# Performance work log

Hardware: AMD Instinct MI355X
Metric: run time of the kernel (lower is better)

## Reference

```python
import jax, jax.numpy as jnp
import numpy as np

B, C, M, NH, F_, W = 2, 8, 8, 8, 1024, 512  # batch, channels, attention_maps, heads, features, frames
HD = F_ // NH
EXP = 4


def _conv(x, w, b):
    y = jax.lax.conv_general_dilated(x, w, (1, 1), 'SAME',
                                     dimension_numbers=('NCHW', 'OIHW', 'NCHW'))
    return y + b[None, :, None, None]


def _rope(x):
    # x: (..., seq, d); lucidrains-style interleaved rotary embedding
    d, n = x.shape[-1], x.shape[-2]
    inv = 1.0 / (10000.0 ** (jnp.arange(0, d, 2, dtype=jnp.float32) / d))
    fr = jnp.repeat(jnp.arange(n, dtype=jnp.float32)[:, None] * inv[None, :], 2, axis=-1)
    cos, sin = jnp.cos(fr), jnp.sin(fr)
    xr = jnp.stack((-x[..., 1::2], x[..., 0::2]), axis=-1).reshape(x.shape)
    return x * cos + xr * sin


def _mcln(x, w, b, eps=1e-5):
    # MultichannelLayerNorm: normalize over features axis (axis=2 of B,C,F,W)
    mu = jnp.mean(x, axis=2, keepdims=True)
    var = jnp.var(x, axis=2, keepdims=True)
    return (x - mu) / jnp.sqrt(var + eps) * w[None, :, :, None] + b[None, :, :, None]


def _mclin(x, w_pw):
    # MultichannelLinear positionwise: per-channel matmul over features
    return jnp.einsum('bcfw,cgf->bcgw', x, w_pw)


def setup_inputs() -> dict:
    key = jax.random.key(0)
    ks = jax.random.split(key, 24)
    s = 0.02
    d = {
        'x': jax.random.normal(ks[0], (B, C, F_, W), jnp.float32),
        'prev_qk': jax.random.normal(ks[1], (B, M, NH, W, W), jnp.float32),
        'qconv_w': jax.random.normal(ks[2], (M, C, 3, 3), jnp.float32) * s,
        'qconv_b': jnp.zeros((M,), jnp.float32),
        'q_pw': jax.random.normal(ks[3], (M, F_, F_), jnp.float32) * s,
        'kconv_w': jax.random.normal(ks[4], (M, C, 3, 3), jnp.float32) * s,
        'kconv_b': jnp.zeros((M,), jnp.float32),
        'k_pw': jax.random.normal(ks[5], (M, F_, F_), jnp.float32) * s,
        'vconv_w': jax.random.normal(ks[6], (M, C, 3, 3), jnp.float32) * s,
        'vconv_b': jnp.zeros((M,), jnp.float32),
        'v_pw': jax.random.normal(ks[7], (M, F_, F_), jnp.float32) * s,
        'o_pw': jax.random.normal(ks[8], (M, F_, F_), jnp.float32) * s,
        'o_dw': jax.random.normal(ks[9], (M, M), jnp.float32) * s,
        'oproj_w': jax.random.normal(ks[10], (C, C + M, 3, 3), jnp.float32) * s,
        'oproj_b': jnp.zeros((C,), jnp.float32),
        'n1_w': jnp.ones((C, F_), jnp.float32),
        'n1_b': jnp.zeros((C, F_), jnp.float32),
        'c1_w': jax.random.normal(ks[11], (C * EXP, C, 3, 3), jnp.float32) * s,
        'c1_b': jnp.zeros((C * EXP,), jnp.float32),
        'c2_w': jax.random.normal(ks[12], (C, C * EXP, 3, 3), jnp.float32) * s,
        'c2_b': jnp.zeros((C,), jnp.float32),
        'n2_w': jnp.ones((C, F_), jnp.float32),
        'n2_b': jnp.zeros((C, F_), jnp.float32),
    }
    return d


def _encoder(x, prev_qk, qconv_w, qconv_b, q_pw, kconv_w, kconv_b, k_pw,
             vconv_w, vconv_b, v_pw, o_pw, o_dw, oproj_w, oproj_b,
             n1_w, n1_b, c1_w, c1_b, c2_w, c2_b, n2_w, n2_b):
    b, c, h, w = x.shape

    def heads(y):  # (B,M,F,W) -> (B,M,NH,W,HD)
        return y.transpose(0, 1, 3, 2).reshape(b, M, w, NH, HD).transpose(0, 1, 3, 2, 4)

    q = _rope(heads(_mclin(_conv(x, qconv_w, qconv_b), q_pw)))
    k = _rope(heads(_mclin(_conv(x, kconv_w, kconv_b), k_pw)))
    v = heads(_mclin(_conv(x, vconv_w, vconv_b), v_pw))

    qk = jnp.einsum('bmnqd,bmnkd->bmnqk', q, k) / jnp.sqrt(jnp.float32(h))
    qk = qk + prev_qk
    a = jnp.einsum('bmnqk,bmnkd->bmnqd', jax.nn.softmax(qk, axis=-1), v)
    a = a.transpose(0, 1, 3, 2, 4).reshape(b, M, w, NH * HD).transpose(0, 1, 3, 2)  # (B,M,F,W)
    a = jnp.einsum('bcfw,dc->bdfw', _mclin(a, o_pw), o_dw)  # depthwise o_linear
    z = _conv(jnp.concatenate((x, a), axis=1), oproj_w, oproj_b)

    hid = _mcln(x + z, n1_w, n1_b)  # dropout is identity in eval
    z2 = _conv(jax.nn.gelu(_conv(hid, c1_w, c1_b), approximate=False), c2_w, c2_b)
    out = _mcln(hid + z2, n2_w, n2_b)
    return out, qk


def reference(x, prev_qk, qconv_w, qconv_b, q_pw, kconv_w, kconv_b, k_pw,
              vconv_w, vconv_b, v_pw, o_pw, o_dw, oproj_w, oproj_b,
              n1_w, n1_b, c1_w, c1_b, c2_w, c2_b, n2_w, n2_b):
    out, qk = _encoder(x, prev_qk, qconv_w, qconv_b, q_pw, kconv_w, kconv_b, k_pw,
                       vconv_w, vconv_b, v_pw, o_pw, o_dw, oproj_w, oproj_b,
                       n1_w, n1_b, c1_w, c1_b, c2_w, c2_b, n2_w, n2_b)
    return (out, out, qk)
```

## Files before the change

### kernel.cpp

```cpp
#include <hip/hip_runtime.h>
#include <math.h>

#define B_ 2
#define C_ 8
#define M_ 8
#define NH_ 8
#define F_ 1024
#define W_ 512
#define HD_ 128
#define FW 524288L
#define PF_ 1026
#define PW_ 514

typedef __bf16 bf16_t;
typedef __bf16 bf16x8 __attribute__((ext_vector_type(8)));
typedef __bf16 bf16x4 __attribute__((ext_vector_type(4)));
typedef float f32x4 __attribute__((ext_vector_type(4)));

__device__ __forceinline__ void gload16(const void* g, void* l) {
    __builtin_amdgcn_global_load_lds(
        (const __attribute__((address_space(1))) unsigned int*)g,
        (__attribute__((address_space(3))) unsigned int*)l,
        16, 0, 0);
}

__device__ __forceinline__ float gelu_f(float v) {
    return 0.5f * v * (1.0f + erff(v * 0.70710678118f));
}

__global__ __launch_bounds__(256)
void pad_stage_k(const float* __restrict__ x, bf16_t* __restrict__ px)
{
    long i = (long)blockIdx.x * 256 + threadIdx.x;
    if (i >= (long)B_ * PF_ * PW_) return;
    int wc = (int)(i % PW_);
    long t = i / PW_;
    int fr = (int)(t % PF_);
    int b  = (int)(t / PF_);
    bf16x8 v = {};
    if (fr >= 1 && fr <= F_ && wc >= 1 && wc <= W_) {
        const float* s = x + (long)b * 8 * FW + (long)(fr - 1) * W_ + (wc - 1);
        #pragma unroll
        for (int c = 0; c < 8; ++c) v[c] = (bf16_t)s[c * FW];
    }
    *(bf16x8*)&px[i * 8] = v;
}

__global__ __launch_bounds__(256)
void borderz8_k(bf16_t* __restrict__ p8a, bf16_t* __restrict__ p8b)
{
    int i = blockIdx.x * 256 + threadIdx.x;
    if (i >= 2 * 3076) return;
    int b = i / 3076, p = i % 3076;
    int fr, wc;
    if (p < 514)       { fr = 0;    wc = p; }
    else if (p < 1028) { fr = 1025; wc = p - 514; }
    else if (p < 2052) { fr = 1 + (p - 1028); wc = 0; }
    else               { fr = 1 + (p - 2052); wc = 513; }
    long pix = ((long)b * PF_ + fr) * PW_ + wc;
    bf16x8 z = {};
    *(bf16x8*)&p8a[pix * 8] = z;
    *(bf16x8*)&p8b[pix * 8] = z;
}

__global__ __launch_bounds__(256)
void borderz32_k(bf16_t* __restrict__ p32)
{
    int i = blockIdx.x * 256 + threadIdx.x;
    if (i >= 2 * 3076) return;
    int b = i / 3076, p = i % 3076;
    int fr, wc;
    if (p < 514)       { fr = 0;    wc = p; }
    else if (p < 1028) { fr = 1025; wc = p - 514; }
    else if (p < 2052) { fr = 1 + (p - 1028); wc = 0; }
    else               { fr = 1 + (p - 2052); wc = 513; }
    long pix = ((long)b * PF_ + fr) * PW_ + wc;
    bf16x8 z = {};
    #pragma unroll
    for (int k = 0; k < 4; ++k) *(bf16x8*)&p32[pix * 32 + k * 8] = z;
}

__global__ void aprep_k(const float* __restrict__ qw, const float* __restrict__ kw,
                        const float* __restrict__ vw, const float* __restrict__ ow,
                        const float* __restrict__ c1w, const float* __restrict__ c2w,
                        const float* __restrict__ qb, const float* __restrict__ kb,
                        const float* __restrict__ vb,
                        bf16_t* __restrict__ a_qkv, bf16_t* __restrict__ a_op,
                        bf16_t* __restrict__ a_c1, bf16_t* __restrict__ a_c2,
                        float* __restrict__ bias_qkv)
{
    int mode = blockIdx.y;
    int i = blockIdx.x * 256 + threadIdx.x;
    if (mode == 0) {
        if (i < 3072) {
            int k = i & 31, co = (i >> 5) & 31, df = i >> 10;
            int tap = k >> 3, ci = k & 7;
            float v = 0.f;
            if (tap < 3) {
                if (co < 8)       v = qw[((co * 8 + ci) * 3 + df) * 3 + tap];
                else if (co < 16) v = kw[(((co - 8) * 8 + ci) * 3 + df) * 3 + tap];
                else if (co < 24) v = vw[(((co - 16) * 8 + ci) * 3 + df) * 3 + tap];
            }
            a_qkv[i] = (bf16_t)v;
        }
        if (i < 32) bias_qkv[i] = (i < 8) ? qb[i] : (i < 16) ? kb[i - 8] : (i < 24) ? vb[i - 16] : 0.f;
    } else if (mode == 1) {
        if (i < 3072) {
            int k = i & 63, co = (i >> 6) & 15, df = i >> 10;
            int src = k >> 5, r = k & 31, tap = r >> 3, ci = src * 8 + (r & 7);
            float v = 0.f;
            if (co < 8 && tap < 3) v = ow[((co * 16 + ci) * 3 + df) * 3 + tap];
            a_op[i] = (bf16_t)v;
        }
    } else if (mode == 2) {
        if (i < 3072) {
            int k = i & 31, co = (i >> 5) & 31, df = i >> 10;
            int tap = k >> 3, ci = k & 7;
            float v = (tap < 3) ? c1w[((co * 8 + ci) * 3 + df) * 3 + tap] : 0.f;
            a_c1[i] = (bf16_t)v;
        }
    } else {
        if (i < 4608) {
            int k = i % 96, co = (i / 96) & 15, df = i / (96 * 16);
            int tap = k >> 5, ci = k & 31;
            float v = (co < 8) ? c2w[((co * 32 + ci) * 3 + df) * 3 + tap] : 0.f;
            a_c2[i] = (bf16_t)v;
        }
    }
}

template<int CIN, int KSTEPS, int MFRAGS, int DUAL, int EPI>
__global__ __launch_bounds__(256)
void convg_k(const bf16_t* __restrict__ px0, const bf16_t* __restrict__ px1,
             const bf16_t* __restrict__ Ab, const float* __restrict__ bias,
             const float* __restrict__ resid, void* __restrict__ outp)
{
    const int f = blockIdx.y, b = blockIdx.z;
    const int tid = threadIdx.x, lane = tid & 63, wid = tid >> 6;
    const int l15 = lane & 15, l4 = lane >> 4;
    const int wbase = blockIdx.x * 256 + wid * 64;
    const int KW = KSTEPS * 32, M16 = MFRAGS * 16;

    bf16x8 af[3][MFRAGS][KSTEPS];
    #pragma unroll
    for (int df = 0; df < 3; ++df)
        #pragma unroll
        for (int mf = 0; mf < MFRAGS; ++mf)
            #pragma unroll
            for (int kk = 0; kk < KSTEPS; ++kk)
                af[df][mf][kk] = *(const bf16x8*)&Ab[(long)(df * M16 + mf * 16 + l15) * KW + kk * 32 + l4 * 8];

    f32x4 acc[MFRAGS][4];
    #pragma unroll
    for (int mf = 0; mf < MFRAGS; ++mf)
        #pragma unroll
        for (int nf = 0; nf < 4; ++nf)
            acc[mf][nf] = (f32x4){0.f, 0.f, 0.f, 0.f};

    #pragma unroll
    for (int df = 0; df < 3; ++df) {
        const long rowb = ((long)(b * PF_ + f + df)) * PW_ * CIN;
        #pragma unroll
        for (int nf = 0; nf < 4; ++nf) {
            const int wp = wbase + nf * 16 + l15;
            #pragma unroll
            for (int kk = 0; kk < KSTEPS; ++kk) {
                const bf16_t* src = (DUAL && kk == 1) ? px1 : px0;
                long addr = (CIN == 8) ? rowb + (long)(wp + l4) * 8
                                       : rowb + (long)(wp + kk) * 32 + l4 * 8;
                bf16x8 bv = *(const bf16x8*)&src[addr];
                #pragma unroll
                for (int mf = 0; mf < MFRAGS; ++mf)
                    acc[mf][nf] = __builtin_amdgcn_mfma_f32_16x16x32_bf16(
                        af[df][mf][kk], bv, acc[mf][nf], 0, 0, 0);
            }
        }
    }

    #pragma unroll
    for (int mf = 0; mf < MFRAGS; ++mf) {
        #pragma unroll
        for (int nf = 0; nf < 4; ++nf) {
            const int wp = wbase + nf * 16 + l15;
            if (EPI == 2) {
                const int cob = mf * 16 + l4 * 4;
                bf16x4 ov;
                #pragma unroll
                for (int r = 0; r < 4; ++r)
                    ov[r] = (bf16_t)gelu_f(acc[mf][nf][r] + bias[cob + r]);
                *(bf16x4*)&((bf16_t*)outp)[(((long)(b * PF_ + f + 1)) * PW_ + wp + 1) * 32 + cob] = ov;
            } else {
                #pragma unroll
                for (int r = 0; r < 4; ++r) {
                    const int co = mf * 16 + l4 * 4 + r;
                    float v = acc[mf][nf][r];
                    if (EPI == 0) {
                        if (co < 24)
                            ((bf16_t*)outp)[((long)(b * 24 + co)) * FW + (long)f * W_ + wp] = (bf16_t)(v + bias[co]);
                    } else {
                        if (co < 8) {
                            long oi = ((long)(b * 8 + co)) * FW + (long)f * W_ + wp;
                            ((bf16_t*)outp)[oi] = (bf16_t)(v + bias[co] + resid[oi]);
                        }
                    }
                }
            }
        }
    }
}

template<int EPI, int OUTBF, int AF32>
__global__ __launch_bounds__(256)
void gemm_mfma_k(const void* __restrict__ Ab_, const bf16_t* __restrict__ Bb,
                 void* __restrict__ Cb, const float* __restrict__ Addb,
                 float scale, int Kdim, int lda, int ldb, int ldc,
                 long sA, long sB, long sC_hi, long sC_lo, int zdivC,
                 long sAdd, int aMod)
{
    __shared__ bf16_t sAt[8192];
    __shared__ bf16_t sBt[8192];

    const int z = blockIdx.z;
    const int m0 = blockIdx.y * 128;
    const int n0 = blockIdx.x * 128;
    const int tid = threadIdx.x;
    const int lane = tid & 63, wid = tid >> 6;
    const int wr = (wid >> 1) * 64, wc = (wid & 1) * 64;
    const int l15 = lane & 15, l4 = lane >> 4;

    const bf16_t* A16 = AF32 ? nullptr : (const bf16_t*)Ab_ + (long)(z % aMod) * sA;
    const float*  A32 = AF32 ? (const float*)Ab_ + (long)(z % aMod) * sA : nullptr;
    const bf16_t* B = Bb + (long)z * sB;

    f32x4 acc[4][4];
    #pragma unroll
    for (int m = 0; m < 4; ++m)
        #pragma unroll
        for (int n = 0; n < 4; ++n)
            acc[m][n] = (f32x4){0.f, 0.f, 0.f, 0.f};

    const int grow = wid * 8 + (lane >> 3);
    const int gslot = lane & 7;
    const int arow = tid >> 1;
    const int akg  = (tid & 1) * 4;

    for (int k0 = 0; k0 < Kdim; k0 += 64) {
        __syncthreads();
        if (AF32) {
            const float* asrc = A32 + (long)(m0 + arow) * lda + k0 + akg * 8;
            const int swz = arow & 7;
            #pragma unroll
            for (int j = 0; j < 4; ++j) {
                float4 u = ((const float4*)asrc)[j * 2];
                float4 v = ((const float4*)asrc)[j * 2 + 1];
                bf16x8 w8 = { (bf16_t)u.x, (bf16_t)u.y, (bf16_t)u.z, (bf16_t)u.w,
                              (bf16_t)v.x, (bf16_t)v.y, (bf16_t)v.z, (bf16_t)v.w };
                *(bf16x8*)&sAt[arow * 64 + (((akg + j) ^ swz) << 3)] = w8;
            }
        } else {
            #pragma unroll
            for (int r = 0; r < 4; ++r) {
                const int row = r * 32 + grow;
                gload16(A16 + (long)(m0 + row) * lda + k0 + ((gslot ^ (row & 7)) << 3),
                        sAt + r * 2048 + wid * 512);
            }
        }
        #pragma unroll
        for (int r = 0; r < 4; ++r) {
            const int row = r * 32 + grow;
            gload16(B + (long)(n0 + row) * ldb + k0 + ((gslot ^ (row & 7)) << 3),
                    sBt + r * 2048 + wid * 512);
        }
        __syncthreads();

        bf16x8 afr[4][2], bfr[4][2];
        #pragma unroll
        for (int m = 0; m < 4; ++m) {
            const int row = wr + m * 16 + l15, swz = row & 7;
            afr[m][0] = *(const bf16x8*)&sAt[row * 64 + ((l4 ^ swz) << 3)];
            afr[m][1] = *(const bf16x8*)&sAt[row * 64 + (((4 + l4) ^ swz) << 3)];
        }
        #pragma unroll
        for (int n = 0; n < 4; ++n) {
            const int row = wc + n * 16 + l15, swz = row & 7;
            bfr[n][0] = *(const bf16x8*)&sBt[row * 64 + ((l4 ^ swz) << 3)];
            bfr[n][1] = *(const bf16x8*)&sBt[row * 64 + (((4 + l4) ^ swz) << 3)];
        }
        #pragma unroll
        for (int kk = 0; kk < 2; ++kk)
            #pragma unroll
            for (int m = 0; m < 4; ++m)
                #pragma unroll
                for (int n = 0; n < 4; ++n)
                    acc[m][n] = __builtin_amdgcn_mfma_f32_16x16x32_bf16(
                        afr[m][kk], bfr[n][kk], acc[m][n], 0, 0, 0);
    }

    if (EPI == 2) {
        #pragma unroll
        for (int m = 0; m < 4; ++m) {
            const int d0 = wr + m * 16 + l4 * 4;
            const float inv0 = __expf(-(float)(d0 >> 1) * 0.14391156507f);
            const float inv1 = __expf(-(float)((d0 >> 1) + 1) * 0.14391156507f);
            #pragma unroll
            for (int n = 0; n < 4; ++n) {
                const int col = n0 + wc + n * 16 + l15;
                float s0, c0, s1, c1;
                __sincosf((float)col * inv0, &s0, &c0);
                __sincosf((float)col * inv1, &s1, &c1);
                float v0 = acc[m][n][0], v1 = acc[m][n][1];
                float v2 = acc[m][n][2], v3 = acc[m][n][3];
                bf16x4 ov = { (bf16_t)(v0 * c0 - v1 * s0), (bf16_t)(v1 * c0 + v0 * s0),
                              (bf16_t)(v2 * c1 - v3 * s1), (bf16_t)(v3 * c1 + v2 * s1) };
                *(bf16x4*)&((bf16_t*)Cb)[(((long)z * 8 + blockIdx.y) * 512 + col) * 128 + d0] = ov;
            }
        }
        return;
    }

    const long zc = (long)(z / zdivC) * sC_hi + (long)(z % zdivC) * sC_lo;
    #pragma unroll
    for (int m = 0; m < 4; ++m) {
        #pragma unroll
        for (int n = 0; n < 4; ++n) {
            #pragma unroll
            for (int r = 0; r < 4; ++r) {
                int row = m0 + wr + m * 16 + l4 * 4 + r;
                int col = n0 + wc + n * 16 + l15;
                float v = acc[m][n][r];
                if (EPI == 1) v = v * scale + Addb[(long)z * sAdd + (long)row * ldc + col];
                long cidx = zc + (long)row * ldc + col;
                if (OUTBF) ((bf16_t*)Cb)[cidx] = (bf16_t)v;
                else       ((float*)Cb)[cidx]  = v;
            }
        }
    }
}

__global__ __launch_bounds__(256)
void tcvt_k(const bf16_t* __restrict__ in, bf16_t* __restrict__ outp)
{
    __shared__ float tile[32][33];
    const int w0 = blockIdx.x * 32, f0 = blockIdx.y * 32;
    const int z = blockIdx.z;
    const int path = z >> 4, bm = z & 15;
    const int inSlice = (bm >> 3) * 24 + path * 8 + (bm & 7);
    const long ibase = (long)inSlice * FW;
    const long obase = (long)z * FW;
    const int tx = threadIdx.x & 31, ty = threadIdx.x >> 5;
    #pragma unroll
    for (int i = 0; i < 4; ++i)
        tile[ty + i * 8][tx] = (float)in[ibase + (long)(f0 + ty + i * 8) * W_ + w0 + tx];
    __syncthreads();
    #pragma unroll
    for (int i = 0; i < 4; ++i)
        outp[obase + (long)(w0 + ty + i * 8) * F_ + f0 + tx] = (bf16_t)tile[tx][ty + i * 8];
}

__device__ inline float waveMax(float v) {
    #pragma unroll
    for (int o = 32; o >= 1; o >>= 1) v = fmaxf(v, __shfl_xor(v, o, 64));
    return v;
}
__device__ inline float waveSum(float v) {
    #pragma unroll
    for (int o = 32; o >= 1; o >>= 1) v += __shfl_xor(v, o, 64);
    return v;
}

__global__ __launch_bounds__(256)
void softmax_k(const float* __restrict__ S, bf16_t* __restrict__ P)
{
    const int wid = threadIdx.x >> 6, lane = threadIdx.x & 63;
    const long row = (long)blockIdx.x * 4 + wid;
    const float4* s4 = (const float4*)(S + row * 512);
    float4 a = s4[lane * 2], b = s4[lane * 2 + 1];
    float m = fmaxf(fmaxf(fmaxf(a.x, a.y), fmaxf(a.z, a.w)),
                    fmaxf(fmaxf(b.x, b.y), fmaxf(b.z, b.w)));
    m = waveMax(m);
    float e0 = __expf(a.x - m), e1 = __expf(a.y - m), e2 = __expf(a.z - m), e3 = __expf(a.w - m);
    float e4 = __expf(b.x - m), e5 = __expf(b.y - m), e6 = __expf(b.z - m), e7 = __expf(b.w - m);
    float su = waveSum(e0 + e1 + e2 + e3 + e4 + e5 + e6 + e7);
    float inv = 1.0f / su;
    bf16x8 o = { (bf16_t)(e0 * inv), (bf16_t)(e1 * inv), (bf16_t)(e2 * inv), (bf16_t)(e3 * inv),
                 (bf16_t)(e4 * inv), (bf16_t)(e5 * inv), (bf16_t)(e6 * inv), (bf16_t)(e7 * inv) };
    *(bf16x8*)(P + row * 512 + lane * 8) = o;
}

__global__ __launch_bounds__(256)
void odw_k(const bf16_t* __restrict__ t, const float* __restrict__ dw, bf16_t* __restrict__ px)
{
    long i = (long)blockIdx.x * 256 + threadIdx.x;
    int w = (int)(i & (W_ - 1));
    long q = i >> 9;
    int f = (int)(q & (F_ - 1));
    int b = (int)(q >> 10);
    const bf16_t* s = t + (long)b * 8 * FW + (long)f * W_ + w;
    float tv[8];
    #pragma unroll
    for (int c = 0; c < 8; ++c) tv[c] = (float)s[c * FW];
    bf16x8 o;
    #pragma unroll
    for (int d = 0; d < 8; ++d) {
        float a = 0.f;
        #pragma unroll
        for (int c = 0; c < 8; ++c) a += tv[c] * dw[d * 8 + c];
        o[d] = (bf16_t)a;
    }
    *(bf16x8*)&px[(((long)b * PF_ + f + 1) * PW_ + w + 1) * 8] = o;
}

template<typename TIN>
__global__ __launch_bounds__(256)
void mcln_k(const TIN* __restrict__ in, const float* __restrict__ gam,
            const float* __restrict__ bet, float* __restrict__ o1, float* __restrict__ o2,
            bf16_t* __restrict__ px)
{
    int wi = threadIdx.x & 31, fg = threadIdx.x >> 5;
    int w0 = blockIdx.x * 32;
    int c = blockIdx.y, b = blockIdx.z;
    long base = ((long)b * C_ + c) * FW + w0 + wi;
    float s = 0.f, q = 0.f;
    for (int f = fg; f < F_; f += 8) {
        float v = (float)in[base + (long)f * W_];
        s += v; q += v * v;
    }
    __shared__ float rs[8][33], rq[8][33];
    __shared__ float mu_s[32], inv_s[32];
    rs[fg][wi] = s; rq[fg][wi] = q;
    __syncthreads();
    if (fg == 0) {
        float ts = 0.f, tq = 0.f;
        for (int g = 0; g < 8; ++g) { ts += rs[g][wi]; tq += rq[g][wi]; }
        float mu = ts * (1.0f / F_);
        float var = tq * (1.0f / F_) - mu * mu;
        mu_s[wi] = mu;
        inv_s[wi] = rsqrtf(var + 1e-5f);
    }
    __syncthreads();
    float mu = mu_s[wi], inv = inv_s[wi];
    for (int f = fg; f < F_; f += 8) {
        float v = (float)in[base + (long)f * W_];
        float r = (v - mu) * inv * gam[c * F_ + f] + bet[c * F_ + f];
        long oi = base + (long)f * W_;
        o1[oi] = r;
        if (o2) o2[oi] = r;
        if (px) px[(((long)b * PF_ + f + 1) * PW_ + (w0 + wi) + 1) * 8 + c] = (bf16_t)r;
    }
}

extern "C" void kernel_launch(void* const* d_in, const int* in_sizes, int n_in,
                              void* d_out, int out_size, void* d_ws, size_t ws_size,
                              hipStream_t stream) {
    (void)in_sizes; (void)n_in; (void)out_size; (void)ws_size;
    const float* x        = (const float*)d_in[0];
    const float* prev_qk  = (const float*)d_in[1];
    const float* qconv_w  = (const float*)d_in[2];
    const float* qconv_b  = (const float*)d_in[3];
    const float* q_pw     = (const float*)d_in[4];
    const float* kconv_w  = (const float*)d_in[5];
    const float* kconv_b  = (const float*)d_in[6];
    const float* k_pw     = (const float*)d_in[7];
    const float* vconv_w  = (const float*)d_in[8];
    const float* vconv_b  = (const float*)d_in[9];
    const float* v_pw     = (const float*)d_in[10];
    const float* o_pw     = (const float*)d_in[11];
    const float* o_dw     = (const float*)d_in[12];
    const float* oproj_w  = (const float*)d_in[13];
    const float* oproj_b  = (const float*)d_in[14];
    const float* n1_w     = (const float*)d_in[15];
    const float* n1_b     = (const float*)d_in[16];
    const float* c1_w     = (const float*)d_in[17];
    const float* c1_b     = (const float*)d_in[18];
    const float* c2_w     = (const float*)d_in[19];
    const float* c2_b     = (const float*)d_in[20];
    const float* n2_w     = (const float*)d_in[21];
    const float* n2_b     = (const float*)d_in[22];

    float* out    = (float*)d_out;
    float* qk_out = out + 16777216L;

    char* wsb = (char*)d_ws;
    bf16_t* PX8  = (bf16_t*)(wsb + 0L);
    bf16_t* XT48 = (bf16_t*)(wsb + 16876032L);
    bf16_t* QR   = (bf16_t*)(wsb + 67207680L);
    bf16_t* KR   = (bf16_t*)(wsb + 83984896L);
    bf16_t* VL   = (bf16_t*)(wsb + 100762112L);
    bf16_t* QKV  = (bf16_t*)(wsb + 117539328L);
    bf16_t* SH   = (bf16_t*)(wsb + 16876032L);
    bf16_t* AT   = (bf16_t*)(wsb + 117539328L);
    bf16_t* F1b  = (bf16_t*)(wsb + 134316544L);
    bf16_t* PXA2 = (bf16_t*)(wsb + 83984896L);
    float*  HID  = (float*) (wsb + 16876032L);
    bf16_t* PXC1 = (bf16_t*)(wsb + 50430464L);
    bf16_t* PRE  = (bf16_t*)(wsb + 151093760L);
    bf16_t* PXH  = (bf16_t*)(wsb + 167870976L);
    bf16_t* ABQ  = (bf16_t*)(wsb + 184748032L);
    bf16_t* ABO  = (bf16_t*)(wsb + 184748032L + 16384L);
    bf16_t* ABC1 = (bf16_t*)(wsb + 184748032L + 32768L);
    bf16_t* ABC2 = (bf16_t*)(wsb + 184748032L + 49152L);
    float*  BQKV = (float*) (wsb + 184748032L + 65536L);

    const dim3 cvgrid(2, F_, B_);
    const dim3 tgrid(16, 32, 48);
    const dim3 ggrid(4, 8, 16);
    const long BIG = 1 << 30;

    aprep_k<<<dim3(18, 4), 256, 0, stream>>>(qconv_w, kconv_w, vconv_w, oproj_w, c1_w, c2_w,
                                             qconv_b, kconv_b, vconv_b,
                                             ABQ, ABO, ABC1, ABC2, BQKV);
    pad_stage_k<<<4121, 256, 0, stream>>>(x, PX8);

    convg_k<8, 1, 2, 0, 0><<<cvgrid, 256, 0, stream>>>(PX8, nullptr, ABQ, BQKV, nullptr, QKV);

    tcvt_k<<<tgrid, 256, 0, stream>>>(QKV, XT48);
    gemm_mfma_k<2, 1, 1><<<ggrid, 256, 0, stream>>>(q_pw, XT48, QR, nullptr, 1.f,
        F_, F_, F_, W_, 1048576L, 524288L, 0L, 0L, 1, 0L, 8);
    gemm_mfma_k<2, 1, 1><<<ggrid, 256, 0, stream>>>(k_pw, XT48 + 16L * FW, KR, nullptr, 1.f,
        F_, F_, F_, W_, 1048576L, 524288L, 0L, 0L, 1, 0L, 8);
    gemm_mfma_k<0, 1, 1><<<ggrid, 256, 0, stream>>>(v_pw, XT48 + 32L * FW, VL, nullptr, 1.f,
        F_, F_, F_, W_, 1048576L, 524288L, 524288L, 0L, 1, 0L, 8);

    gemm_mfma_k<1, 0, 0><<<dim3(4, 4, 128), 256, 0, stream>>>(QR, KR, qk_out, prev_qk,
        0.03125f, HD_, HD_, HD_, W_, 65536L, 65536L, 262144L, 0L, 1, 262144L, (int)BIG);
    softmax_k<<<16384, 256, 0, stream>>>(qk_out, SH);
    gemm_mfma_k<0, 1, 0><<<dim3(1, 4, 128), 256, 0, stream>>>(SH, VL, AT, nullptr, 1.f,
        W_, W_, W_, F_, 262144L, 65536L, 524288L, 128L, 8, 0L, (int)BIG);

    gemm_mfma_k<0, 1, 1><<<ggrid, 256, 0, stream>>>(o_pw, AT, F1b, nullptr, 1.f,
        F_, F_, F_, W_, 1048576L, 524288L, 524288L, 0L, 1, 0L, 8);
    odw_k<<<4096, 256, 0, stream>>>(F1b, o_dw, PXA2);
    borderz8_k<<<25, 256, 0, stream>>>(PXA2, PXH);

    convg_k<8, 2, 1, 1, 1><<<cvgrid, 256, 0, stream>>>(PX8, PXA2, ABO, oproj_b, x, PRE);
    borderz32_k<<<25, 256, 0, stream>>>(PXC1);

    mcln_k<bf16_t><<<dim3(16, 8, 2), 256, 0, stream>>>(PRE, n1_w, n1_b, HID, nullptr, PXH);

    convg_k<8, 1, 2, 0, 2><<<cvgrid, 256, 0, stream>>>(PXH, nullptr, ABC1, c1_b, nullptr, PXC1);
    convg_k<32, 3, 1, 0, 1><<<cvgrid, 256, 0, stream>>>(PXC1, nullptr, ABC2, c2_b, HID, PRE);
    mcln_k<bf16_t><<<dim3(16, 8, 2), 256, 0, stream>>>(PRE, n2_w, n2_b, out, out + 8388608L, nullptr);
}
```

Before: 706.1 us.

## Fuse softmax into PV GEMM, merge QKV GEMMs and border-zero kernels

Replaces the standalone softmax kernel and the separate P·V GEMM with one kernel. It computes row max and sum from the fp32 scores, exponentiates tiles into LDS as bf16, and applies the 1/sum scale in the epilogue. This avoids writing and re-reading the bf16 probability matrix. The three Q/K/V projection GEMM launches are merged into one 48-slice launch, and the two border-zero kernels into one. The fused kernel reads the score matrix twice and recomputes the exponentials, and the normalization now happens after accumulation rather than before bf16 rounding.

```diff
diff --git a/kernel.cpp b/kernel.cpp
--- a/kernel.cpp
+++ b/kernel.cpp
@@ -47,7 +47,7 @@
 }
 
 __global__ __launch_bounds__(256)
-void borderz8_k(bf16_t* __restrict__ p8a, bf16_t* __restrict__ p8b)
+void borderz_all_k(bf16_t* __restrict__ p8a, bf16_t* __restrict__ p8b, bf16_t* __restrict__ p32)
 {
     int i = blockIdx.x * 256 + threadIdx.x;
     if (i >= 2 * 3076) return;
@@ -61,21 +61,6 @@
     bf16x8 z = {};
     *(bf16x8*)&p8a[pix * 8] = z;
     *(bf16x8*)&p8b[pix * 8] = z;
-}
-
-__global__ __launch_bounds__(256)
-void borderz32_k(bf16_t* __restrict__ p32)
-{
-    int i = blockIdx.x * 256 + threadIdx.x;
-    if (i >= 2 * 3076) return;
-    int b = i / 3076, p = i % 3076;
-    int fr, wc;
-    if (p < 514)       { fr = 0;    wc = p; }
-    else if (p < 1028) { fr = 1025; wc = p - 514; }
-    else if (p < 2052) { fr = 1 + (p - 1028); wc = 0; }
-    else               { fr = 1 + (p - 2052); wc = 513; }
-    long pix = ((long)b * PF_ + fr) * PW_ + wc;
-    bf16x8 z = {};
     #pragma unroll
     for (int k = 0; k < 4; ++k) *(bf16x8*)&p32[pix * 32 + k * 8] = z;
 }
@@ -296,7 +281,103 @@
                         afr[m][kk], bfr[n][kk], acc[m][n], 0, 0, 0);
     }
 
-    if (EPI == 2) {
+    const long zc = (long)(z / zdivC) * sC_hi + (long)(z % zdivC) * sC_lo;
+    #pragma unroll
+    for (int m = 0; m < 4; ++m) {
+        #pragma unroll
+        for (int n = 0; n < 4; ++n) {
+            #pragma unroll
+            for (int r = 0; r < 4; ++r) {
+                int row = m0 + wr + m * 16 + l4 * 4 + r;
+                int col = n0 + wc + n * 16 + l15;
+                float v = acc[m][n][r];
+                if (EPI == 1) v = v * scale + Addb[(long)z * sAdd + (long)row * ldc + col];
+                long cidx = zc + (long)row * ldc + col;
+                if (OUTBF) ((bf16_t*)Cb)[cidx] = (bf16_t)v;
+                else       ((float*)Cb)[cidx]  = v;
+            }
+        }
+    }
+}
+
+__global__ __launch_bounds__(256)
+void qkvgemm_k(const float* __restrict__ qw, const float* __restrict__ kw,
+               const float* __restrict__ vw, const bf16_t* __restrict__ XT,
+               bf16_t* __restrict__ outp )
+{
+    __shared__ bf16_t sAt[8192];
+    __shared__ bf16_t sBt[8192];
+
+    const int zz = blockIdx.z;
+    const int path = zz >> 4, bm = zz & 15;
+    const float* A32 = ((path == 0) ? qw : (path == 1) ? kw : vw) + (long)(bm & 7) * 1048576L;
+    const bf16_t* B = XT + (long)zz * FW;
+    const int m0 = blockIdx.y * 128;
+    const int n0 = blockIdx.x * 128;
+    const int tid = threadIdx.x;
+    const int lane = tid & 63, wid = tid >> 6;
+    const int wr = (wid >> 1) * 64, wc = (wid & 1) * 64;
+    const int l15 = lane & 15, l4 = lane >> 4;
+
+    f32x4 acc[4][4];
+    #pragma unroll
+    for (int m = 0; m < 4; ++m)
+        #pragma unroll
+        for (int n = 0; n < 4; ++n)
+            acc[m][n] = (f32x4){0.f, 0.f, 0.f, 0.f};
+
+    const int grow = wid * 8 + (lane >> 3);
+    const int gslot = lane & 7;
+    const int arow = tid >> 1;
+    const int akg  = (tid & 1) * 4;
+
+    for (int k0 = 0; k0 < 1024; k0 += 64) {
+        __syncthreads();
+        {
+            const float* asrc = A32 + (long)(m0 + arow) * 1024 + k0 + akg * 8;
+            const int swz = arow & 7;
+            #pragma unroll
+            for (int j = 0; j < 4; ++j) {
+                float4 u = ((const float4*)asrc)[j * 2];
+                float4 v = ((const float4*)asrc)[j * 2 + 1];
+                bf16x8 w8 = { (bf16_t)u.x, (bf16_t)u.y, (bf16_t)u.z, (bf16_t)u.w,
+                              (bf16_t)v.x, (bf16_t)v.y, (bf16_t)v.z, (bf16_t)v.w };
+                *(bf16x8*)&sAt[arow * 64 + (((akg + j) ^ swz) << 3)] = w8;
+            }
+        }
+        #pragma unroll
+        for (int r = 0; r < 4; ++r) {
+            const int row = r * 32 + grow;
+            gload16(B + (long)(n0 + row) * 1024 + k0 + ((gslot ^ (row & 7)) << 3),
+                    sBt + r * 2048 + wid * 512);
+        }
+        __syncthreads();
+
+        bf16x8 afr[4][2], bfr[4][2];
+        #pragma unroll
+        for (int m = 0; m < 4; ++m) {
+            const int row = wr + m * 16 + l15, swz = row & 7;
+            afr[m][0] = *(const bf16x8*)&sAt[row * 64 + ((l4 ^ swz) << 3)];
+            afr[m][1] = *(const bf16x8*)&sAt[row * 64 + (((4 + l4) ^ swz) << 3)];
+        }
+        #pragma unroll
+        for (int n = 0; n < 4; ++n) {
+            const int row = wc + n * 16 + l15, swz = row & 7;
+            bfr[n][0] = *(const bf16x8*)&sBt[row * 64 + ((l4 ^ swz) << 3)];
+            bfr[n][1] = *(const bf16x8*)&sBt[row * 64 + (((4 + l4) ^ swz) << 3)];
+        }
+        #pragma unroll
+        for (int kk = 0; kk < 2; ++kk)
+            #pragma unroll
+            for (int m = 0; m < 4; ++m)
+                #pragma unroll
+                for (int n = 0; n < 4; ++n)
+                    acc[m][n] = __builtin_amdgcn_mfma_f32_16x16x32_bf16(
+                        afr[m][kk], bfr[n][kk], acc[m][n], 0, 0, 0);
+    }
+
+    if (path < 2) {
+        const long base = (long)path * 8388608L + (((long)bm * 8 + blockIdx.y) * 512L) * 128L;
         #pragma unroll
         for (int m = 0; m < 4; ++m) {
             const int d0 = wr + m * 16 + l4 * 4;
@@ -312,26 +393,130 @@
                 float v2 = acc[m][n][2], v3 = acc[m][n][3];
                 bf16x4 ov = { (bf16_t)(v0 * c0 - v1 * s0), (bf16_t)(v1 * c0 + v0 * s0),
                               (bf16_t)(v2 * c1 - v3 * s1), (bf16_t)(v3 * c1 + v2 * s1) };
-                *(bf16x4*)&((bf16_t*)Cb)[(((long)z * 8 + blockIdx.y) * 512 + col) * 128 + d0] = ov;
-            }
-        }
-        return;
-    }
-
-    const long zc = (long)(z / zdivC) * sC_hi + (long)(z % zdivC) * sC_lo;
+                *(bf16x4*)&outp[base + (long)col * 128 + d0] = ov;
+            }
+        }
+    } else {
+        const long base = 16777216L + (long)bm * FW;
+        #pragma unroll
+        for (int m = 0; m < 4; ++m)
+            #pragma unroll
+            for (int n = 0; n < 4; ++n)
+                #pragma unroll
+                for (int r = 0; r < 4; ++r) {
+                    int row = m0 + wr + m * 16 + l4 * 4 + r;
+                    int col = n0 + wc + n * 16 + l15;
+                    outp[base + (long)row * 512 + col] = (bf16_t)acc[m][n][r];
+                }
+    }
+}
+
+__global__ __launch_bounds__(256)
+void smpv_k(const float* __restrict__ S, const bf16_t* __restrict__ VL,
+            bf16_t* __restrict__ AT)
+{
+    __shared__ bf16_t sP[8192];
+    __shared__ bf16_t sB[8192];
+    __shared__ float smax[128], sinv[128];
+
+    const int z = blockIdx.z;
+    const int m0 = blockIdx.x * 128;
+    const float* Sb = S + (long)z * 262144L;
+    const bf16_t* Bb = VL + (long)z * 65536L;
+    const int tid = threadIdx.x, lane = tid & 63, wid = tid >> 6;
+    const int l15 = lane & 15, l4 = lane >> 4;
+    const int wr = (wid >> 1) * 64, wc = (wid & 1) * 64;
+
+    {
+        const int g = lane >> 4;
+        for (int i = 0; i < 8; ++i) {
+            const int row = i * 16 + wid * 4 + g;
+            const float4* sr = (const float4*)(Sb + (long)(m0 + row) * 512);
+            float4 v[8];
+            #pragma unroll
+            for (int j = 0; j < 8; ++j) v[j] = sr[l15 + j * 16];
+            float mx = -1e30f;
+            #pragma unroll
+            for (int j = 0; j < 8; ++j)
+                mx = fmaxf(mx, fmaxf(fmaxf(v[j].x, v[j].y), fmaxf(v[j].z, v[j].w)));
+            #pragma unroll
+            for (int o = 1; o <= 8; o <<= 1) mx = fmaxf(mx, __shfl_xor(mx, o, 64));
+            float s = 0.f;
+            #pragma unroll
+            for (int j = 0; j < 8; ++j)
+                s += __expf(v[j].x - mx) + __expf(v[j].y - mx) +
+                     __expf(v[j].z - mx) + __expf(v[j].w - mx);
+            #pragma unroll
+            for (int o = 1; o <= 8; o <<= 1) s += __shfl_xor(s, o, 64);
+            if (l15 == 0) { smax[row] = mx; sinv[row] = 1.0f / s; }
+        }
+    }
+    __syncthreads();
+
+    f32x4 acc[4][4];
+    #pragma unroll
+    for (int m = 0; m < 4; ++m)
+        #pragma unroll
+        for (int n = 0; n < 4; ++n)
+            acc[m][n] = (f32x4){0.f, 0.f, 0.f, 0.f};
+
+    const int grow = wid * 8 + (lane >> 3);
+    const int gslot = lane & 7;
+    const int prow0 = tid >> 4, pl = tid & 15;
+
+    for (int kt = 0; kt < 512; kt += 64) {
+        __syncthreads();
+        #pragma unroll
+        for (int p = 0; p < 8; ++p) {
+            const int row = p * 16 + prow0;
+            float4 v = *(const float4*)(Sb + (long)(m0 + row) * 512 + kt + pl * 4);
+            float mr = smax[row];
+            bf16x4 e = { (bf16_t)__expf(v.x - mr), (bf16_t)__expf(v.y - mr),
+                         (bf16_t)__expf(v.z - mr), (bf16_t)__expf(v.w - mr) };
+            *(bf16x4*)((char*)sP + row * 128 + ((((pl >> 1) ^ (row & 7))) << 4) + (pl & 1) * 8) = e;
+        }
+        #pragma unroll
+        for (int r = 0; r < 4; ++r) {
+            const int row = r * 32 + grow;
+            gload16(Bb + (long)row * 512 + kt + ((gslot ^ (row & 7)) << 3),
+                    sB + r * 2048 + wid * 512);
+        }
+        __syncthreads();
+
+        bf16x8 afr[4][2], bfr[4][2];
+        #pragma unroll
+        for (int m = 0; m < 4; ++m) {
+            const int row = wr + m * 16 + l15, swz = row & 7;
+            afr[m][0] = *(const bf16x8*)&sP[row * 64 + ((l4 ^ swz) << 3)];
+            afr[m][1] = *(const bf16x8*)&sP[row * 64 + (((4 + l4) ^ swz) << 3)];
+        }
+        #pragma unroll
+        for (int n = 0; n < 4; ++n) {
+            const int row = wc + n * 16 + l15, swz = row & 7;
+            bfr[n][0] = *(const bf16x8*)&sB[row * 64 + ((l4 ^ swz) << 3)];
+            bfr[n][1] = *(const bf16x8*)&sB[row * 64 + (((4 + l4) ^ swz) << 3)];
+        }
+        #pragma unroll
+        for (int kk = 0; kk < 2; ++kk)
+            #pragma unroll
+            for (int m = 0; m < 4; ++m)
+                #pragma unroll
+                for (int n = 0; n < 4; ++n)
+                    acc[m][n] = __builtin_amdgcn_mfma_f32_16x16x32_bf16(
+                        afr[m][kk], bfr[n][kk], acc[m][n], 0, 0, 0);
+    }
+
+    const long base = (long)(z >> 3) * FW + (long)(z & 7) * 128L;
     #pragma unroll
     for (int m = 0; m < 4; ++m) {
         #pragma unroll
         for (int n = 0; n < 4; ++n) {
             #pragma unroll
             for (int r = 0; r < 4; ++r) {
-                int row = m0 + wr + m * 16 + l4 * 4 + r;
-                int col = n0 + wc + n * 16 + l15;
-                float v = acc[m][n][r];
-                if (EPI == 1) v = v * scale + Addb[(long)z * sAdd + (long)row * ldc + col];
-                long cidx = zc + (long)row * ldc + col;
-                if (OUTBF) ((bf16_t*)Cb)[cidx] = (bf16_t)v;
-                else       ((float*)Cb)[cidx]  = v;
+                const int row = wr + m * 16 + l4 * 4 + r;
+                const int col = wc + n * 16 + l15;
+                float v = acc[m][n][r] * sinv[row];
+                AT[base + (long)(m0 + row) * 1024 + col] = (bf16_t)v;
             }
         }
     }
@@ -355,36 +540,6 @@
     #pragma unroll
     for (int i = 0; i < 4; ++i)
         outp[obase + (long)(w0 + ty + i * 8) * F_ + f0 + tx] = (bf16_t)tile[tx][ty + i * 8];
-}
-
-__device__ inline float waveMax(float v) {
-    #pragma unroll
-    for (int o = 32; o >= 1; o >>= 1) v = fmaxf(v, __shfl_xor(v, o, 64));
-    return v;
-}
-__device__ inline float waveSum(float v) {
-    #pragma unroll
-    for (int o = 32; o >= 1; o >>= 1) v += __shfl_xor(v, o, 64);
-    return v;
-}
-
-__global__ __launch_bounds__(256)
-void softmax_k(const float* __restrict__ S, bf16_t* __restrict__ P)
-{
-    const int wid = threadIdx.x >> 6, lane = threadIdx.x & 63;
-    const long row = (long)blockIdx.x * 4 + wid;
-    const float4* s4 = (const float4*)(S + row * 512);
-    float4 a = s4[lane * 2], b = s4[lane * 2 + 1];
-    float m = fmaxf(fmaxf(fmaxf(a.x, a.y), fmaxf(a.z, a.w)),
-                    fmaxf(fmaxf(b.x, b.y), fmaxf(b.z, b.w)));
-    m = waveMax(m);
-    float e0 = __expf(a.x - m), e1 = __expf(a.y - m), e2 = __expf(a.z - m), e3 = __expf(a.w - m);
-    float e4 = __expf(b.x - m), e5 = __expf(b.y - m), e6 = __expf(b.z - m), e7 = __expf(b.w - m);
-    float su = waveSum(e0 + e1 + e2 + e3 + e4 + e5 + e6 + e7);
-    float inv = 1.0f / su;
-    bf16x8 o = { (bf16_t)(e0 * inv), (bf16_t)(e1 * inv), (bf16_t)(e2 * inv), (bf16_t)(e3 * inv),
-                 (bf16_t)(e4 * inv), (bf16_t)(e5 * inv), (bf16_t)(e6 * inv), (bf16_t)(e7 * inv) };
-    *(bf16x8*)(P + row * 512 + lane * 8) = o;
 }
 
 __global__ __launch_bounds__(256)
@@ -487,7 +642,6 @@
     bf16_t* KR   = (bf16_t*)(wsb + 83984896L);
     bf16_t* VL   = (bf16_t*)(wsb + 100762112L);
     bf16_t* QKV  = (bf16_t*)(wsb + 117539328L);
-    bf16_t* SH   = (bf16_t*)(wsb + 16876032L);
     bf16_t* AT   = (bf16_t*)(wsb + 117539328L);
     bf16_t* F1b  = (bf16_t*)(wsb + 134316544L);
     bf16_t* PXA2 = (bf16_t*)(wsb + 83984896L);
@@ -503,7 +657,6 @@
 
     const dim3 cvgrid(2, F_, B_);
     const dim3 tgrid(16, 32, 48);
-    const dim3 ggrid(4, 8, 16);
     const long BIG = 1 << 30;
 
     aprep_k<<<dim3(18, 4), 256, 0, stream>>>(qconv_w, kconv_w, vconv_w, oproj_w, c1_w, c2_w,
@@ -514,26 +667,18 @@
     convg_k<8, 1, 2, 0, 0><<<cvgrid, 256, 0, stream>>>(PX8, nullptr, ABQ, BQKV, nullptr, QKV);
 
     tcvt_k<<<tgrid, 256, 0, stream>>>(QKV, XT48);
-    gemm_mfma_k<2, 1, 1><<<ggrid, 256, 0, stream>>>(q_pw, XT48, QR, nullptr, 1.f,
-        F_, F_, F_, W_, 1048576L, 524288L, 0L, 0L, 1, 0L, 8);
-    gemm_mfma_k<2, 1, 1><<<ggrid, 256, 0, stream>>>(k_pw, XT48 + 16L * FW, KR, nullptr, 1.f,
-        F_, F_, F_, W_, 1048576L, 524288L, 0L, 0L, 1, 0L, 8);
-    gemm_mfma_k<0, 1, 1><<<ggrid, 256, 0, stream>>>(v_pw, XT48 + 32L * FW, VL, nullptr, 1.f,
-        F_, F_, F_, W_, 1048576L, 524288L, 524288L, 0L, 1, 0L, 8);
+    qkvgemm_k<<<dim3(4, 8, 48), 256, 0, stream>>>(q_pw, k_pw, v_pw, XT48, QR);
 
     gemm_mfma_k<1, 0, 0><<<dim3(4, 4, 128), 256, 0, stream>>>(QR, KR, qk_out, prev_qk,
         0.03125f, HD_, HD_, HD_, W_, 65536L, 65536L, 262144L, 0L, 1, 262144L, (int)BIG);
-    softmax_k<<<16384, 256, 0, stream>>>(qk_out, SH);
-    gemm_mfma_k<0, 1, 0><<<dim3(1, 4, 128), 256, 0, stream>>>(SH, VL, AT, nullptr, 1.f,
-        W_, W_, W_, F_, 262144L, 65536L, 524288L, 128L, 8, 0L, (int)BIG);
-
-    gemm_mfma_k<0, 1, 1><<<ggrid, 256, 0, stream>>>(o_pw, AT, F1b, nullptr, 1.f,
+    smpv_k<<<dim3(4, 1, 128), 256, 0, stream>>>(qk_out, VL, AT);
+
+    gemm_mfma_k<0, 1, 1><<<dim3(4, 8, 16), 256, 0, stream>>>(o_pw, AT, F1b, nullptr, 1.f,
         F_, F_, F_, W_, 1048576L, 524288L, 524288L, 0L, 1, 0L, 8);
     odw_k<<<4096, 256, 0, stream>>>(F1b, o_dw, PXA2);
-    borderz8_k<<<25, 256, 0, stream>>>(PXA2, PXH);
+    borderz_all_k<<<25, 256, 0, stream>>>(PXA2, PXH, PXC1);
 
     convg_k<8, 2, 1, 1, 1><<<cvgrid, 256, 0, stream>>>(PX8, PXA2, ABO, oproj_b, x, PRE);
-    borderz32_k<<<25, 256, 0, stream>>>(PXC1);
 
     mcln_k<bf16_t><<<dim3(16, 8, 2), 256, 0, stream>>>(PRE, n1_w, n1_b, HID, nullptr, PXH);
 
```

New measurement: 695.0 us. Within noise of the previous version (-1.6%).
